# Performance work log

Hardware: AMD Instinct MI355X
Metric: run time of the kernel (lower is better)

Reference implementation:

```python
import jax, jax.numpy as jnp
import numpy as np

B, T, H, NH = 4, 2048, 1024, 16
HD = H // NH  # 64


def setup_inputs() -> dict:
    key = jax.random.key(0)
    ks = jax.random.split(key, 8)
    s = 0.02
    return {
        "hidden_states": jax.random.normal(ks[0], (B, T, H), dtype=jnp.float32),
        "attention_mask": jnp.zeros((B, 1, 1, T), dtype=jnp.float32),
        "Wq": jax.random.normal(ks[1], (H, H), dtype=jnp.float32) * s,
        "bq": jnp.zeros((H,), dtype=jnp.float32),
        "Wk": jax.random.normal(ks[2], (H, H), dtype=jnp.float32) * s,
        "bk": jnp.zeros((H,), dtype=jnp.float32),
        "Wv": jax.random.normal(ks[3], (H, H), dtype=jnp.float32) * s,
        "bv": jnp.zeros((H,), dtype=jnp.float32),
    }


def _split_heads(x):
    # [B, T, H] -> [B, NH, T, HD]
    b, t, _ = x.shape
    return x.reshape(b, t, NH, HD).transpose(0, 2, 1, 3)


def reference(hidden_states, attention_mask, Wq, bq, Wk, bk, Wv, bv):
    # QKV projections (torch Linear: x @ W.T + b)
    q = _split_heads(hidden_states @ Wq.T + bq)
    k = _split_heads(hidden_states @ Wk.T + bk)
    v = _split_heads(hidden_states @ Wv.T + bv)

    scale = HD ** (-0.5)
    # [B, NH, T, T]
    scores = jnp.einsum("bhqd,bhkd->bhqk", q, k) * scale
    t = q.shape[2]
    causal = jnp.triu(jnp.ones((t, t), dtype=bool), k=1)
    scores = jnp.where(causal[None, None], -jnp.inf, scores)
    scores = scores + attention_mask  # additive mask [B,1,1,T]
    probs = jax.nn.softmax(scores, axis=-1)
    # dropout is identity in eval mode
    out = jnp.einsum("bhqk,bhkd->bhqd", probs, v)
    # [B, NH, T, HD] -> [B, T, H]
    return out.transpose(0, 2, 1, 3).reshape(hidden_states.shape[0], t, H)
```

## Files before the change

kernel.cpp:

```cpp
#include <hip/hip_runtime.h>
#include <math.h>

#define B_  4
#define T_  2048
#define H_  1024
#define NH_ 16
#define HD_ 64

typedef __bf16  bf16x8  __attribute__((ext_vector_type(8)));
typedef float   f32x4   __attribute__((ext_vector_type(4)));
typedef unsigned short ushort8v __attribute__((ext_vector_type(8)));
typedef short   short4v __attribute__((ext_vector_type(4)));

__device__ __forceinline__ unsigned short f2bf(float f) {
    unsigned int u = __builtin_bit_cast(unsigned int, f);
    u += 0x7fffu + ((u >> 16) & 1u);
    return (unsigned short)(u >> 16);
}

__device__ __forceinline__ f32x4 mfma16x16x16bf16(short4v a, short4v b, f32x4 c) {
#if __has_builtin(__builtin_amdgcn_mfma_f32_16x16x16bf16_1k)
    return __builtin_amdgcn_mfma_f32_16x16x16bf16_1k(a, b, c, 0, 0, 0);
#else
    f32x4 d = c;
    asm volatile("v_mfma_f32_16x16x16_bf16 %0, %1, %2, %0\n\ts_nop 7\n\ts_nop 7"
                 : "+v"(d) : "v"(a), "v"(b));
    return d;
#endif
}

__device__ __forceinline__ void gload_lds16(const unsigned short* g,
                                            unsigned short* l) {
    __builtin_amdgcn_global_load_lds(
        (const __attribute__((address_space(1))) unsigned int*)g,
        (__attribute__((address_space(3))) unsigned int*)l, 16, 0, 0);
}

__global__ void cvt_f32_bf16(const float* __restrict__ in,
                             unsigned short* __restrict__ out, int n8) {
    int stride = gridDim.x * blockDim.x;
    for (int i = blockIdx.x * blockDim.x + threadIdx.x; i < n8; i += stride) {
        const float4* p = reinterpret_cast<const float4*>(in) + (size_t)i * 2;
        float4 f0 = p[0], f1 = p[1];
        ushort8v o;
        o[0] = f2bf(f0.x); o[1] = f2bf(f0.y); o[2] = f2bf(f0.z); o[3] = f2bf(f0.w);
        o[4] = f2bf(f1.x); o[5] = f2bf(f1.y); o[6] = f2bf(f1.z); o[7] = f2bf(f1.w);
        reinterpret_cast<ushort8v*>(out)[i] = o;
    }
}

__global__ void cvt_w3(const float* __restrict__ Wq, const float* __restrict__ Wk,
                       const float* __restrict__ Wv,
                       unsigned short* __restrict__ oq, unsigned short* __restrict__ ok,
                       unsigned short* __restrict__ ov, int n8) {
    const int z = blockIdx.y;
    const float* in = (z == 0) ? Wq : (z == 1) ? Wk : Wv;
    unsigned short* out = (z == 0) ? oq : (z == 1) ? ok : ov;
    int stride = gridDim.x * blockDim.x;
    for (int i = blockIdx.x * blockDim.x + threadIdx.x; i < n8; i += stride) {
        const float4* p = reinterpret_cast<const float4*>(in) + (size_t)i * 2;
        float4 f0 = p[0], f1 = p[1];
        ushort8v o;
        o[0] = f2bf(f0.x); o[1] = f2bf(f0.y); o[2] = f2bf(f0.z); o[3] = f2bf(f0.w);
        o[4] = f2bf(f1.x); o[5] = f2bf(f1.y); o[6] = f2bf(f1.z); o[7] = f2bf(f1.w);
        reinterpret_cast<ushort8v*>(out)[i] = o;
    }
}

__global__ __launch_bounds__(256) void qkv_gemm_all(
    const unsigned short* __restrict__ X,
    const unsigned short* __restrict__ Wq,
    const unsigned short* __restrict__ Wk,
    const unsigned short* __restrict__ Wv,
    const float* __restrict__ bq,
    const float* __restrict__ bk,
    const float* __restrict__ bv,
    unsigned short* __restrict__ Qo,
    unsigned short* __restrict__ Ko,
    unsigned short* __restrict__ Vo)
{
    const int id     = blockIdx.x;
    const int xcd    = id & 7;
    const int within = id >> 3;
    const int z      = within >> 6;
    const int rest   = within & 63;
    const int xb     = rest >> 3;
    const int yb     = xcd * 8 + (rest & 7);

    const unsigned short* W = (z == 0) ? Wq : (z == 1) ? Wk : Wv;
    const float* bias = (z == 0) ? bq : (z == 1) ? bk : bv;
    unsigned short* out = (z == 0) ? Qo : (z == 1) ? Ko : Vo;

    const int K = 1024;
    const int t    = threadIdx.x;
    const int lane = t & 63;
    const int wid  = t >> 6;
    const int lo = lane & 15, hi = lane >> 4;
    const int wm = wid >> 1, wn = wid & 1;
    const int m0 = yb * 128;
    const int n0 = xb * 128;

    __shared__ unsigned short As[2][128 * 64];
    __shared__ unsigned short Bs[2][128 * 64];

    const int srowoff = lane >> 3;
    const int scol    = lane & 7;

    f32x4 acc[4][4];
#pragma unroll
    for (int i = 0; i < 4; ++i)
#pragma unroll
        for (int j = 0; j < 4; ++j) acc[i][j] = (f32x4){0.f, 0.f, 0.f, 0.f};

#define STAGE_(AS, BS, KOFF)                                                  \
    do {                                                                      \
        _Pragma("unroll") for (int p = 0; p < 4; ++p) {                       \
            const int rowb = p * 32 + wid * 8;                                \
            const int row  = rowb + srowoff;                                  \
            const int c16  = scol ^ (row & 7);                                \
            gload_lds16(&X[(size_t)(m0 + row) * K + (KOFF) + c16 * 8],        \
                        &(AS)[rowb * 64]);                                    \
            gload_lds16(&W[(size_t)(n0 + row) * K + (KOFF) + c16 * 8],        \
                        &(BS)[rowb * 64]);                                    \
        }                                                                     \
    } while (0)

#define COMPUTE_(AS, BS)                                                      \
    do {                                                                      \
        _Pragma("unroll") for (int ks = 0; ks < 2; ++ks) {                    \
            bf16x8 a[4], b[4];                                                \
            _Pragma("unroll") for (int mt = 0; mt < 4; ++mt) {                \
                const int row = wm * 64 + mt * 16 + lo;                       \
                a[mt] = *reinterpret_cast<const bf16x8*>(                     \
                    &(AS)[row * 64 + (((ks * 4 + hi) ^ (lo & 7)) * 8)]);      \
            }                                                                 \
            _Pragma("unroll") for (int nt = 0; nt < 4; ++nt) {                \
                const int row = wn * 64 + nt * 16 + lo;                       \
                b[nt] = *reinterpret_cast<const bf16x8*>(                     \
                    &(BS)[row * 64 + (((ks * 4 + hi) ^ (lo & 7)) * 8)]);      \
            }                                                                 \
            _Pragma("unroll") for (int mt = 0; mt < 4; ++mt)                  \
                _Pragma("unroll") for (int nt = 0; nt < 4; ++nt)              \
                    acc[mt][nt] = __builtin_amdgcn_mfma_f32_16x16x32_bf16(    \
                        a[mt], b[nt], acc[mt][nt], 0, 0, 0);                  \
        }                                                                     \
    } while (0)

    STAGE_(As[0], Bs[0], 0);
    __syncthreads();
#pragma unroll
    for (int k0 = 0; k0 < K; k0 += 128) {
        STAGE_(As[1], Bs[1], k0 + 64);
        COMPUTE_(As[0], Bs[0]);
        __syncthreads();
        if (k0 + 128 < K) STAGE_(As[0], Bs[0], k0 + 128);
        COMPUTE_(As[1], Bs[1]);
        __syncthreads();
    }

#pragma unroll
    for (int nt = 0; nt < 4; ++nt) {
        int n = n0 + wn * 64 + nt * 16 + lo;
        float bv_ = bias[n];
        int h = n >> 6, d = n & 63;
#pragma unroll
        for (int mt = 0; mt < 4; ++mt) {
            int mbase = m0 + wm * 64 + mt * 16 + hi * 4;
            int bb = mbase >> 11;
            int tt = mbase & 2047;
            size_t tilebase = ((size_t)(bb * NH_ + h) * 32 + (tt >> 6)) * 4096;
            if (z == 2) {
                ushort4 pk;
                pk.x = f2bf(acc[mt][nt][0] + bv_);
                pk.y = f2bf(acc[mt][nt][1] + bv_);
                pk.z = f2bf(acc[mt][nt][2] + bv_);
                pk.w = f2bf(acc[mt][nt][3] + bv_);
                *reinterpret_cast<ushort4*>(
                    &out[tilebase + (size_t)mt * 1024 + (size_t)(hi * 16 + lo) * 16 + nt * 4]) = pk;
            } else if (z == 1) {
                const int ksd = d >> 5;
                const int hif = (d >> 3) & 3;
                const int jd  = d & 7;
                size_t fragbase = tilebase + (size_t)(mt * 2 + ksd) * 512;
#pragma unroll
                for (int r = 0; r < 4; ++r)
                    out[fragbase + (size_t)(hif * 16 + hi * 4 + r) * 8 + jd] =
                        f2bf(acc[mt][nt][r] + bv_);
            } else {
                size_t base = (size_t)(bb * NH_ + h) * T_;
#pragma unroll
                for (int r = 0; r < 4; ++r)
                    out[(base + tt + r) * HD_ + d] = f2bf(acc[mt][nt][r] + bv_);
            }
        }
    }
#undef STAGE_
#undef COMPUTE_
}

__global__ __launch_bounds__(128, 2) void attn_fwd15(
    const unsigned short* __restrict__ Q,
    const unsigned short* __restrict__ Kf,
    const unsigned short* __restrict__ Vf,
    const float* __restrict__ amask,
    float* __restrict__ out)
{
    const float SC    = 0.125f * 1.44269504089f;
    const float LOG2E = 1.44269504089f;

    const int lane = threadIdx.x & 63;
    const int w    = threadIdx.x >> 6;
    const int lo = lane & 15, hi = lane >> 4;

    const int bid    = blockIdx.x;
    const int xcd    = bid & 7;
    const int within = bid >> 3;
    const int bh     = xcd * 8 + (within & 7);
    const int u      = 63 - (within >> 3);
    const int b      = bh >> 4;
    const int h      = bh & 15;

    const unsigned short* Qg = Q + (size_t)bh * T_ * HD_;
    const float* am = amask + (size_t)b * T_;
    float* outBase = out + (size_t)b * T_ * H_ + h * HD_;

    __shared__ f32x4 Lo[2][4][64];
    __shared__ float Ll[2][64];

    const int q0   = u * 32;
    const int nt   = (u >> 1) + 1;
    const int half = nt >> 1;
    const int ktBeg = w ? half : 0;
    const int ktEnd = w ? nt : half;

    bf16x8 qf[2][2];
#pragma unroll
    for (int mt = 0; mt < 2; ++mt)
#pragma unroll
        for (int ks = 0; ks < 2; ++ks)
            qf[mt][ks] = *reinterpret_cast<const bf16x8*>(
                &Qg[(size_t)(q0 + mt * 16 + lo) * HD_ + ks * 32 + hi * 8]);

    f32x4 o[2][4];
#pragma unroll
    for (int mt = 0; mt < 2; ++mt)
#pragma unroll
        for (int dt = 0; dt < 4; ++dt) o[mt][dt] = (f32x4){0.f, 0.f, 0.f, 0.f};
    float l_r[2] = {0.f, 0.f};

    const unsigned short* kp = Kf + ((size_t)bh * 32 + ktBeg) * 4096;
    const unsigned short* vp = Vf + ((size_t)bh * 32 + ktBeg) * 4096;
    const float*          ap = am + ktBeg * 64;

    for (int kt = ktBeg; kt < ktEnd; ++kt, kp += 4096, vp += 4096, ap += 64) {
        const int kv0 = kt * 64;

        bf16x8 kf[4][2];
#pragma unroll
        for (int ct = 0; ct < 4; ++ct)
#pragma unroll
            for (int ks = 0; ks < 2; ++ks)
                kf[ct][ks] = *reinterpret_cast<const bf16x8*>(
                    &kp[(ct * 2 + ks) * 512 + lane * 8]);

        short4v vf[4][4];
#pragma unroll
        for (int ct = 0; ct < 4; ++ct) {
            union { ushort8v u8; short4v s4[2]; } va, vb;
            va.u8 = *reinterpret_cast<const ushort8v*>(&vp[ct * 1024 + lane * 16]);
            vb.u8 = *reinterpret_cast<const ushort8v*>(&vp[ct * 1024 + lane * 16 + 8]);
            vf[0][ct] = va.s4[0];
            vf[1][ct] = va.s4[1];
            vf[2][ct] = vb.s4[0];
            vf[3][ct] = vb.s4[1];
        }

        f32x4 amv[4];
#pragma unroll
        for (int ct = 0; ct < 4; ++ct)
            amv[ct] = *reinterpret_cast<const f32x4*>(&ap[ct * 16 + hi * 4]) * LOG2E;

        f32x4 s[2][4];
#pragma unroll
        for (int mt = 0; mt < 2; ++mt)
#pragma unroll
            for (int ct = 0; ct < 4; ++ct) s[mt][ct] = (f32x4){0.f, 0.f, 0.f, 0.f};
#pragma unroll
        for (int ks = 0; ks < 2; ++ks)
#pragma unroll
            for (int ct = 0; ct < 4; ++ct)
#pragma unroll
                for (int mt = 0; mt < 2; ++mt)
                    s[mt][ct] = __builtin_amdgcn_mfma_f32_16x16x32_bf16(
                        kf[ct][ks], qf[mt][ks], s[mt][ct], 0, 0, 0);

        const bool edge = (kv0 + 63 > q0);

        short4v p[2][4];
#pragma unroll
        for (int mt = 0; mt < 2; ++mt) {
            f32x4 rsv = (f32x4){0.f, 0.f, 0.f, 0.f};
#pragma unroll
            for (int ct = 0; ct < 4; ++ct) {
                f32x4 sv;
#pragma unroll
                for (int r = 0; r < 4; ++r)
                    sv[r] = fmaf(s[mt][ct][r], SC, amv[ct][r]);
                if (edge) {
                    const int q = q0 + mt * 16 + lo;
#pragma unroll
                    for (int r = 0; r < 4; ++r)
                        if (kv0 + ct * 16 + hi * 4 + r > q) sv[r] = -INFINITY;
                }
                short4v pk;
#pragma unroll
                for (int r = 0; r < 4; ++r) {
                    float pe = exp2f(sv[r]);
                    rsv[r] += pe;
                    __bf16 hb = (__bf16)pe;
                    pk[r] = __builtin_bit_cast(short, hb);
                }
                p[mt][ct] = pk;
            }
            l_r[mt] += (rsv[0] + rsv[1]) + (rsv[2] + rsv[3]);
        }

#pragma unroll
        for (int ct = 0; ct < 4; ++ct)
#pragma unroll
            for (int mt = 0; mt < 2; ++mt)
#pragma unroll
                for (int dt = 0; dt < 4; ++dt)
                    o[mt][dt] = mfma16x16x16bf16(vf[dt][ct], p[mt][ct], o[mt][dt]);
    }

    if (w == 1) {
#pragma unroll
        for (int mt = 0; mt < 2; ++mt) {
            Ll[mt][lane] = l_r[mt];
#pragma unroll
            for (int dt = 0; dt < 4; ++dt)
                Lo[mt][dt][lane] = o[mt][dt];
        }
    }
    __syncthreads();
    if (w == 0) {
#pragma unroll
        for (int mt = 0; mt < 2; ++mt) {
            float lf = l_r[mt] + Ll[mt][lane];
            lf += __shfl_xor(lf, 16, 64);
            lf += __shfl_xor(lf, 32, 64);
            const float inv = 1.0f / lf;
            const int tq = q0 + mt * 16 + lo;
            float* orow = outBase + (size_t)tq * H_;
#pragma unroll
            for (int dt = 0; dt < 4; ++dt) {
                f32x4 v = (o[mt][dt] + Lo[mt][dt][lane]) * inv;
                *reinterpret_cast<f32x4*>(&orow[dt * 16 + hi * 4]) = v;
            }
        }
    }
}

extern "C" void kernel_launch(void* const* d_in, const int* in_sizes, int n_in,
                              void* d_out, int out_size, void* d_ws, size_t ws_size,
                              hipStream_t stream) {
    const float* hs    = (const float*)d_in[0];
    const float* amask = (const float*)d_in[1];
    const float* Wq    = (const float*)d_in[2];
    const float* bq    = (const float*)d_in[3];
    const float* Wk    = (const float*)d_in[4];
    const float* bk    = (const float*)d_in[5];
    const float* Wv    = (const float*)d_in[6];
    const float* bv    = (const float*)d_in[7];
    float* out = (float*)d_out;

    unsigned short* Xbf = (unsigned short*)d_ws;
    unsigned short* Wqb = Xbf + (size_t)8192 * 1024;
    unsigned short* Wkb = Wqb + (size_t)1024 * 1024;
    unsigned short* Wvb = Wkb + (size_t)1024 * 1024;
    unsigned short* Qb  = Wvb + (size_t)1024 * 1024;
    unsigned short* Kfb = Qb  + (size_t)B_ * NH_ * T_ * HD_;
    unsigned short* Vfb = Kfb + (size_t)B_ * NH_ * T_ * HD_;

    cvt_f32_bf16<<<4096, 256, 0, stream>>>(hs, Xbf, (8192 * 1024) / 8);
    dim3 gw(512, 3);
    cvt_w3<<<gw, 256, 0, stream>>>(Wq, Wk, Wv, Wqb, Wkb, Wvb, (1024 * 1024) / 8);

    qkv_gemm_all<<<1536, 256, 0, stream>>>(Xbf, Wqb, Wkb, Wvb, bq, bk, bv,
                                           Qb, Kfb, Vfb);

    attn_fwd15<<<4096, 128, 0, stream>>>(Qb, Kfb, Vfb, amask, out);
}
```

Baseline: 154.3 us.

## Enlarge QKV GEMM tile to 256x128 with 8 waves and explicit waitcnt pipelining

The QKV projection GEMM now uses 512-thread blocks computing 256x128 output tiles, which halves the grid and increases reuse of the weight tile. The K loop is restructured so each k-tile loads its fragments to registers, hits a raw s_barrier, then issues the next global-to-LDS prefetch into the same buffer, runs MFMAs at raised priority, and waits with partial vmcnt. The aim is to overlap global loads with compute and cut synchronization overhead. It adds hand-written waitcnt and barrier logic and fixes the output index math for the new tile layout, which is fragile if the count assumptions are wrong.

```diff
diff --git a/kernel.cpp b/kernel.cpp
--- a/kernel.cpp
+++ b/kernel.cpp
@@ -35,6 +35,11 @@
         (const __attribute__((address_space(1))) unsigned int*)g,
         (__attribute__((address_space(3))) unsigned int*)l, 16, 0, 0);
 }
+
+#define SBARRIER()   asm volatile("s_barrier" ::: "memory")
+#define LGKMCNT0()   asm volatile("s_waitcnt lgkmcnt(0)" ::: "memory")
+#define VMCNT6()     asm volatile("s_waitcnt vmcnt(6)" ::: "memory")
+#define VMCNT0()     asm volatile("s_waitcnt vmcnt(0)" ::: "memory")
 
 __global__ void cvt_f32_bf16(const float* __restrict__ in,
                              unsigned short* __restrict__ out, int n8) {
@@ -67,7 +72,7 @@
     }
 }
 
-__global__ __launch_bounds__(256) void qkv_gemm_all(
+__global__ __launch_bounds__(512) void qkv_gemm_all(
     const unsigned short* __restrict__ X,
     const unsigned short* __restrict__ Wq,
     const unsigned short* __restrict__ Wk,
@@ -82,10 +87,10 @@
     const int id     = blockIdx.x;
     const int xcd    = id & 7;
     const int within = id >> 3;
-    const int z      = within >> 6;
-    const int rest   = within & 63;
-    const int xb     = rest >> 3;
-    const int yb     = xcd * 8 + (rest & 7);
+    const int z      = within >> 5;
+    const int rest   = within & 31;
+    const int xb     = rest & 7;
+    const int yb     = xcd * 4 + (rest >> 3);
 
     const unsigned short* W = (z == 0) ? Wq : (z == 1) ? Wk : Wv;
     const float* bias = (z == 0) ? bq : (z == 1) ? bk : bv;
@@ -97,10 +102,10 @@
     const int wid  = t >> 6;
     const int lo = lane & 15, hi = lane >> 4;
     const int wm = wid >> 1, wn = wid & 1;
-    const int m0 = yb * 128;
+    const int m0 = yb * 256;
     const int n0 = xb * 128;
 
-    __shared__ unsigned short As[2][128 * 64];
+    __shared__ unsigned short As[2][256 * 64];
     __shared__ unsigned short Bs[2][128 * 64];
 
     const int srowoff = lane >> 3;
@@ -115,47 +120,60 @@
 #define STAGE_(AS, BS, KOFF)                                                  \
     do {                                                                      \
         _Pragma("unroll") for (int p = 0; p < 4; ++p) {                       \
-            const int rowb = p * 32 + wid * 8;                                \
+            const int rowb = p * 64 + wid * 8;                                \
             const int row  = rowb + srowoff;                                  \
             const int c16  = scol ^ (row & 7);                                \
             gload_lds16(&X[(size_t)(m0 + row) * K + (KOFF) + c16 * 8],        \
                         &(AS)[rowb * 64]);                                    \
+        }                                                                     \
+        _Pragma("unroll") for (int p = 0; p < 2; ++p) {                       \
+            const int rowb = p * 64 + wid * 8;                                \
+            const int row  = rowb + srowoff;                                  \
+            const int c16  = scol ^ (row & 7);                                \
             gload_lds16(&W[(size_t)(n0 + row) * K + (KOFF) + c16 * 8],        \
                         &(BS)[rowb * 64]);                                    \
         }                                                                     \
     } while (0)
 
-#define COMPUTE_(AS, BS)                                                      \
+#define KTILE_(AS, BS, HAVE_NEXT, KOFF_NEXT)                                  \
     do {                                                                      \
-        _Pragma("unroll") for (int ks = 0; ks < 2; ++ks) {                    \
-            bf16x8 a[4], b[4];                                                \
-            _Pragma("unroll") for (int mt = 0; mt < 4; ++mt) {                \
-                const int row = wm * 64 + mt * 16 + lo;                       \
-                a[mt] = *reinterpret_cast<const bf16x8*>(                     \
-                    &(AS)[row * 64 + (((ks * 4 + hi) ^ (lo & 7)) * 8)]);      \
-            }                                                                 \
-            _Pragma("unroll") for (int nt = 0; nt < 4; ++nt) {                \
-                const int row = wn * 64 + nt * 16 + lo;                       \
-                b[nt] = *reinterpret_cast<const bf16x8*>(                     \
-                    &(BS)[row * 64 + (((ks * 4 + hi) ^ (lo & 7)) * 8)]);      \
-            }                                                                 \
-            _Pragma("unroll") for (int mt = 0; mt < 4; ++mt)                  \
-                _Pragma("unroll") for (int nt = 0; nt < 4; ++nt)              \
-                    acc[mt][nt] = __builtin_amdgcn_mfma_f32_16x16x32_bf16(    \
-                        a[mt], b[nt], acc[mt][nt], 0, 0, 0);                  \
-        }                                                                     \
+        bf16x8 a[4][2], bfr[4][2];                                            \
+        _Pragma("unroll") for (int mt = 0; mt < 4; ++mt)                      \
+            _Pragma("unroll") for (int ks = 0; ks < 2; ++ks)                  \
+                a[mt][ks] = *reinterpret_cast<const bf16x8*>(                 \
+                    &(AS)[(wm * 64 + mt * 16 + lo) * 64 +                     \
+                          (((ks * 4 + hi) ^ (lo & 7)) * 8)]);                 \
+        _Pragma("unroll") for (int nt = 0; nt < 4; ++nt)                      \
+            _Pragma("unroll") for (int ks = 0; ks < 2; ++ks)                  \
+                bfr[nt][ks] = *reinterpret_cast<const bf16x8*>(               \
+                    &(BS)[(wn * 64 + nt * 16 + lo) * 64 +                     \
+                          (((ks * 4 + hi) ^ (lo & 7)) * 8)]);                 \
+        LGKMCNT0();                                                           \
+        SBARRIER();                     \
+        if (HAVE_NEXT) STAGE_(AS, BS, KOFF_NEXT);      \
+        __builtin_amdgcn_s_setprio(1);                                        \
+        _Pragma("unroll") for (int mt = 0; mt < 4; ++mt)                      \
+            _Pragma("unroll") for (int nt = 0; nt < 4; ++nt)                  \
+                acc[mt][nt] = __builtin_amdgcn_mfma_f32_16x16x32_bf16(        \
+                    a[mt][0], bfr[nt][0], acc[mt][nt], 0, 0, 0);              \
+        _Pragma("unroll") for (int mt = 0; mt < 4; ++mt)                      \
+            _Pragma("unroll") for (int nt = 0; nt < 4; ++nt)                  \
+                acc[mt][nt] = __builtin_amdgcn_mfma_f32_16x16x32_bf16(        \
+                    a[mt][1], bfr[nt][1], acc[mt][nt], 0, 0, 0);              \
+        __builtin_amdgcn_s_setprio(0);                                        \
+        if (HAVE_NEXT) VMCNT6(); else VMCNT0();                               \
+        SBARRIER();                          \
     } while (0)
 
     STAGE_(As[0], Bs[0], 0);
-    __syncthreads();
+    STAGE_(As[1], Bs[1], 64);
+    VMCNT6();
+    SBARRIER();
+
 #pragma unroll
     for (int k0 = 0; k0 < K; k0 += 128) {
-        STAGE_(As[1], Bs[1], k0 + 64);
-        COMPUTE_(As[0], Bs[0]);
-        __syncthreads();
-        if (k0 + 128 < K) STAGE_(As[0], Bs[0], k0 + 128);
-        COMPUTE_(As[1], Bs[1]);
-        __syncthreads();
+        KTILE_(As[0], Bs[0], (k0 + 128 < K), k0 + 128);
+        KTILE_(As[1], Bs[1], (k0 + 192 < K), k0 + 192);
     }
 
 #pragma unroll
@@ -168,6 +186,7 @@
             int mbase = m0 + wm * 64 + mt * 16 + hi * 4;
             int bb = mbase >> 11;
             int tt = mbase & 2047;
+            int ct = (tt >> 4) & 3;
             size_t tilebase = ((size_t)(bb * NH_ + h) * 32 + (tt >> 6)) * 4096;
             if (z == 2) {
                 ushort4 pk;
@@ -176,12 +195,12 @@
                 pk.z = f2bf(acc[mt][nt][2] + bv_);
                 pk.w = f2bf(acc[mt][nt][3] + bv_);
                 *reinterpret_cast<ushort4*>(
-                    &out[tilebase + (size_t)mt * 1024 + (size_t)(hi * 16 + lo) * 16 + nt * 4]) = pk;
+                    &out[tilebase + (size_t)ct * 1024 + (size_t)(hi * 16 + lo) * 16 + nt * 4]) = pk;
             } else if (z == 1) {
                 const int ksd = d >> 5;
                 const int hif = (d >> 3) & 3;
                 const int jd  = d & 7;
-                size_t fragbase = tilebase + (size_t)(mt * 2 + ksd) * 512;
+                size_t fragbase = tilebase + (size_t)(ct * 2 + ksd) * 512;
 #pragma unroll
                 for (int r = 0; r < 4; ++r)
                     out[fragbase + (size_t)(hif * 16 + hi * 4 + r) * 8 + jd] =
@@ -195,7 +214,7 @@
         }
     }
 #undef STAGE_
-#undef COMPUTE_
+#undef KTILE_
 }
 
 __global__ __launch_bounds__(128, 2) void attn_fwd15(
@@ -387,8 +406,8 @@
     dim3 gw(512, 3);
     cvt_w3<<<gw, 256, 0, stream>>>(Wq, Wk, Wv, Wqb, Wkb, Wvb, (1024 * 1024) / 8);
 
-    qkv_gemm_all<<<1536, 256, 0, stream>>>(Xbf, Wqb, Wkb, Wvb, bq, bk, bv,
-                                           Qb, Kfb, Vfb);
+    qkv_gemm_all<<<768, 512, 0, stream>>>(Xbf, Wqb, Wkb, Wvb, bq, bk, bv,
+                                          Qb, Kfb, Vfb);
 
     attn_fwd15<<<4096, 128, 0, stream>>>(Qb, Kfb, Vfb, amask, out);
 }
```

Result: no change. 153.8 us (-0.3%).
